# Kernel tuning notes

Hardware: AMD Instinct MI355X
Metric: run time of the kernel (lower is better)

Reference implementation:

```python
import jax, jax.numpy as jnp
import numpy as np

N = 100000   # nodes
E = 1000000  # edges
F_IN = 64    # input node features
EMB = 32     # init_emb
C = 32       # hidden/out channels per head
H = 4        # heads
HC = H * C   # 128
NEG_SLOPE = 0.2


def setup_inputs() -> dict:
    key = jax.random.key(0)
    ks = jax.random.split(key, 40)
    g = lambda k, shape: jax.random.normal(k, shape, jnp.float32) * 0.05
    inp = {
        "x": jax.random.normal(ks[0], (N, F_IN), jnp.float32),
        "edge_index": jax.random.randint(ks[1], (2, E), 0, N, jnp.int32),
        "W0": g(ks[2], (F_IN, EMB)),
    }
    i = 3
    for p, din in (("f", EMB), ("m", HC), ("l", HC)):
        inp[p + "_Wl"] = g(ks[i], (din, HC)); i += 1
        inp[p + "_bl"] = g(ks[i], (HC,));     i += 1
        inp[p + "_Wr"] = g(ks[i], (din, HC)); i += 1
        inp[p + "_br"] = g(ks[i], (HC,));     i += 1
        inp[p + "_att"] = g(ks[i], (H, C));   i += 1
        inp[p + "_cb"] = g(ks[i], (HC,));     i += 1
        inp[p + "_Ws"] = g(ks[i], (din, HC)); i += 1
        inp[p + "_bs"] = g(ks[i], (HC,));     i += 1
    return inp


def _gatv2(x, src, dst, Wl, bl, Wr, br, att, cb):
    # GATv2Conv, bipartite weights, concat heads, add_self_loops=False
    xl = (x @ Wl + bl).reshape(-1, H, C)  # source transform [N,H,C]
    xr = (x @ Wr + br).reshape(-1, H, C)  # target transform [N,H,C]
    e = xl[src] + xr[dst]                 # [E,H,C]
    s = jnp.where(e > 0, e, NEG_SLOPE * e)
    score = jnp.einsum('ehc,hc->eh', s, att)  # [E,H]
    mmax = jax.ops.segment_max(score, dst, num_segments=N)
    ex = jnp.exp(score - mmax[dst])
    den = jax.ops.segment_sum(ex, dst, num_segments=N)
    alpha = ex / den[dst]                 # segment softmax over in-edges
    out = jax.ops.segment_sum(xl[src] * alpha[:, :, None], dst, num_segments=N)
    return out.reshape(-1, HC) + cb


def reference(x, edge_index,
              W0,
              f_Wl, f_bl, f_Wr, f_br, f_att, f_cb, f_Ws, f_bs,
              m_Wl, m_bl, m_Wr, m_br, m_att, m_cb, m_Ws, m_bs,
              l_Wl, l_bl, l_Wr, l_br, l_att, l_cb, l_Ws, l_bs):
    src, dst = edge_index[0], edge_index[1]
    h = jax.nn.relu(x @ W0)
    h = jax.nn.relu(_gatv2(h, src, dst, f_Wl, f_bl, f_Wr, f_br, f_att, f_cb) + h @ f_Ws + f_bs)
    for _ in range(3):  # conv_mid / lin_mid weights are SHARED across the 3 iterations
        h = jax.nn.relu(_gatv2(h, src, dst, m_Wl, m_bl, m_Wr, m_br, m_att, m_cb) + h @ m_Ws + m_bs)
    h = _gatv2(h, src, dst, l_Wl, l_bl, l_Wr, l_br, l_att, l_cb) + h @ l_Ws + l_bs
    h = h / jnp.linalg.norm(h, axis=-1, keepdims=True)
    return h
```

## Files before the change

### kernel.cpp

```cpp
#include <hip/hip_runtime.h>
#include <hip/hip_bf16.h>
#include <math.h>

#define N_NODES 100000
#define N_EDGES 1000000
#define NEG_SLOPE 0.2f
#define NBUCK 98
#define BSHIFT 10
#define SLAB 12288
#define BINA_EDGES 4096

typedef short v8s __attribute__((ext_vector_type(8)));
typedef float v4f __attribute__((ext_vector_type(4)));

__device__ inline unsigned pack_bf16(float a, float b) {
    unsigned ua = __float_as_uint(a);
    unsigned ub = __float_as_uint(b);
    ua = (ua + 0x7FFFu + ((ua >> 16) & 1u)) >> 16;
    ub = (ub + 0x7FFFu + ((ub >> 16) & 1u)) >> 16;
    return ua | (ub << 16);
}
__device__ inline unsigned short bf16_rn(float x) {
    unsigned u = __float_as_uint(x);
    u = (u + 0x7FFFu + ((u >> 16) & 1u)) >> 16;
    return (unsigned short)u;
}
__device__ inline void unpack8(uint4 u, float* f) {
    f[0] = __uint_as_float(u.x << 16); f[1] = __uint_as_float(u.x & 0xFFFF0000u);
    f[2] = __uint_as_float(u.y << 16); f[3] = __uint_as_float(u.y & 0xFFFF0000u);
    f[4] = __uint_as_float(u.z << 16); f[5] = __uint_as_float(u.z & 0xFFFF0000u);
    f[6] = __uint_as_float(u.w << 16); f[7] = __uint_as_float(u.w & 0xFFFF0000u);
}

__global__ void init_cursors(int* __restrict__ gcursor) {
    int t = blockIdx.x * blockDim.x + threadIdx.x;
    if (t < NBUCK) gcursor[t] = t * SLAB;
}

__global__ __launch_bounds__(256) void binA_kernel(
    const int* __restrict__ src, const int* __restrict__ dst,
    int* __restrict__ gcursor, int* __restrict__ tmp) {
    __shared__ int bstart[NBUCK];
    __shared__ int addrbase[NBUCK];
    __shared__ int bcur[NBUCK];
    __shared__ int s[256];
    __shared__ int staged_val[BINA_EDGES];
    __shared__ int staged_addr[BINA_EDGES];
    const int tid = threadIdx.x;
    const int base = blockIdx.x * BINA_EDGES;
    const int ecount = min(BINA_EDGES, N_EDGES - base);

    if (tid < NBUCK) bcur[tid] = 0;
    __syncthreads();
    for (int j = tid; j < ecount; j += 256) {
        int d = dst[base + j];
        atomicAdd(&bcur[d >> BSHIFT], 1);
    }
    __syncthreads();
    int own = (tid < NBUCK) ? bcur[tid] : 0;
    s[tid] = own;
    __syncthreads();
    for (int off = 1; off < 256; off <<= 1) {
        int u = (tid >= off) ? s[tid - off] : 0;
        __syncthreads();
        s[tid] += u;
        __syncthreads();
    }
    if (tid < NBUCK) {
        int excl = s[tid] - own;
        bstart[tid] = excl;
        int resv = atomicAdd(&gcursor[tid], own);
        addrbase[tid] = resv - excl;
    }
    __syncthreads();
    if (tid < NBUCK) bcur[tid] = bstart[tid];
    __syncthreads();
    for (int j = tid; j < ecount; j += 256) {
        int d = dst[base + j];
        int sr = src[base + j];
        int bk = d >> BSHIFT;
        int lpos = atomicAdd(&bcur[bk], 1);
        staged_val[lpos] = ((d & ((1 << BSHIFT) - 1)) << 17) | sr;
        staged_addr[lpos] = addrbase[bk] + lpos;
    }
    __syncthreads();
    for (int j = tid; j < ecount; j += 256)
        tmp[staged_addr[j]] = staged_val[j];
}

__global__ void bucket_scan(const int* __restrict__ gcursor, int* __restrict__ bbase,
                            int* __restrict__ row_ptr) {
    __shared__ int s[128];
    int t = threadIdx.x;
    int v = (t < NBUCK) ? (gcursor[t] - t * SLAB) : 0;
    s[t] = v;
    __syncthreads();
    for (int off = 1; off < 128; off <<= 1) {
        int u = (t >= off) ? s[t - off] : 0;
        __syncthreads();
        s[t] += u;
        __syncthreads();
    }
    if (t < NBUCK) bbase[t] = s[t] - v;
    if (t == 0) row_ptr[N_NODES] = N_EDGES;
}

__global__ __launch_bounds__(256) void binB_kernel(
    const int* __restrict__ tmp, const int* __restrict__ gcursor,
    const int* __restrict__ bbase, int* __restrict__ row_ptr,
    int* __restrict__ srcs) {
    __shared__ int hist[1024];
    __shared__ int tsum[256];
    const int b = blockIdx.x;
    const int tid = threadIdx.x;
    const int base = b * SLAB;
    const int cnt = gcursor[b] - base;
    const int node0 = b << BSHIFT;
    const int nodes_in = min(1024, N_NODES - node0);
    const int gb = bbase[b];

    for (int i = tid; i < 1024; i += 256) hist[i] = 0;
    __syncthreads();
    for (int i = tid; i < cnt; i += 256)
        atomicAdd(&hist[tmp[base + i] >> 17], 1);
    __syncthreads();
    int v[4], local = 0;
#pragma unroll
    for (int j = 0; j < 4; ++j) {
        v[j] = hist[tid * 4 + j];
        local += v[j];
    }
    tsum[tid] = local;
    __syncthreads();
    for (int off = 1; off < 256; off <<= 1) {
        int u = (tid >= off) ? tsum[tid - off] : 0;
        __syncthreads();
        tsum[tid] += u;
        __syncthreads();
    }
    int run = tsum[tid] - local;
#pragma unroll
    for (int j = 0; j < 4; ++j) {
        hist[tid * 4 + j] = run;
        run += v[j];
    }
    __syncthreads();
    for (int i = tid; i < nodes_in; i += 256)
        row_ptr[node0 + i] = gb + hist[i];
    __syncthreads();
    for (int i = tid; i < cnt; i += 256) {
        int e = tmp[base + i];
        int pos = atomicAdd(&hist[e >> 17], 1);
        srcs[gb + pos] = e & 0x1FFFF;
    }
}

template <int K>
__global__ void convert_w(const float* __restrict__ Wl, const float* __restrict__ Wr,
                          const float* __restrict__ Ws, unsigned short* __restrict__ wt) {
    int idx = blockIdx.x * blockDim.x + threadIdx.x;
    if (idx >= 384 * K) return;
    int n = idx / K;
    int k = idx - n * K;
    int sec = n >> 7;
    int nn = n & 127;
    const float* W = (sec == 0) ? Wl : (sec == 1) ? Wr : Ws;
    wt[idx] = bf16_rn(W[k * 128 + nn]);
}

__global__ void h0_kernel(const float* __restrict__ x, const float* __restrict__ W0,
                          unsigned short* __restrict__ h) {
    int tid = blockIdx.x * blockDim.x + threadIdx.x;
    int col = tid & 31;
    int row = tid >> 5;
    if (row >= N_NODES) return;
    const float* xr = x + row * 64;
    float acc = 0.f;
#pragma unroll
    for (int k = 0; k < 64; ++k) acc = fmaf(xr[k], W0[k * 32 + col], acc);
    h[row * 32 + col] = bf16_rn(fmaxf(acc, 0.f));
}

template <int K>
__global__ __launch_bounds__(256) void mm3_mfma(
    const unsigned short* __restrict__ A, const unsigned short* __restrict__ Wt,
    const float* __restrict__ bl, const float* __restrict__ br, const float* __restrict__ bs,
    const float* __restrict__ cb,
    unsigned short* __restrict__ xl_bf, unsigned short* __restrict__ xr_bf,
    unsigned short* __restrict__ sk_bf) {
    const int tid = threadIdx.x;
    const int wave = tid >> 6;
    const int lane = tid & 63;
    const int q = lane >> 4;
    const int li = lane & 15;
    const int r0 = blockIdx.x * 256 + wave * 64;
    constexpr int KS = K / 32;

    v8s a[4][KS];
#pragma unroll
    for (int mi = 0; mi < 4; ++mi) {
        int row = r0 + mi * 16 + li;
        row = row < N_NODES ? row : N_NODES - 1;
#pragma unroll
        for (int ks = 0; ks < KS; ++ks)
            a[mi][ks] = *(const v8s*)&A[(size_t)row * K + ks * 32 + q * 8];
    }

    for (int t = 0; t < 6; ++t) {
        const int sec = t >> 1;
        const int c0 = (t & 1) * 64;
        v4f acc[4][4];
#pragma unroll
        for (int mi = 0; mi < 4; ++mi)
#pragma unroll
            for (int ni = 0; ni < 4; ++ni) acc[mi][ni] = (v4f)(0.f);

#pragma unroll
        for (int ks = 0; ks < KS; ++ks) {
            v8s b[4];
#pragma unroll
            for (int ni = 0; ni < 4; ++ni) {
                int col = sec * 128 + c0 + ni * 16 + li;
                b[ni] = *(const v8s*)&Wt[(size_t)col * K + ks * 32 + q * 8];
            }
#pragma unroll
            for (int mi = 0; mi < 4; ++mi)
#pragma unroll
                for (int ni = 0; ni < 4; ++ni)
                    acc[mi][ni] = __builtin_amdgcn_mfma_f32_16x16x32_bf16(b[ni], a[mi][ks], acc[mi][ni], 0, 0, 0);
        }

        unsigned short* dstp = (sec == 0) ? xl_bf : (sec == 1) ? xr_bf : sk_bf;
#pragma unroll
        for (int ni = 0; ni < 4; ++ni) {
            int cbase = c0 + ni * 16 + q * 4;
            float4 b4;
            if (sec == 0) b4 = *(const float4*)&bl[cbase];
            else if (sec == 1) b4 = *(const float4*)&br[cbase];
            else {
                float4 t1 = *(const float4*)&bs[cbase];
                float4 t2 = *(const float4*)&cb[cbase];
                b4 = make_float4(t1.x + t2.x, t1.y + t2.y, t1.z + t2.z, t1.w + t2.w);
            }
#pragma unroll
            for (int mi = 0; mi < 4; ++mi) {
                int row = r0 + mi * 16 + li;
                if (row >= N_NODES) continue;
                v4f v = acc[mi][ni];
                uint2 pk;
                pk.x = pack_bf16(v[0] + b4.x, v[1] + b4.y);
                pk.y = pack_bf16(v[2] + b4.z, v[3] + b4.w);
                *(uint2*)&dstp[(size_t)row * 128 + cbase] = pk;
            }
        }
    }
}

__global__ __launch_bounds__(256) void agg_kernel(
    const uint4* __restrict__ xlb4, const uint4* __restrict__ xrb4,
    const uint4* __restrict__ skb4, const int* __restrict__ row_ptr,
    const int* __restrict__ srcs, const float* __restrict__ att,
    uint4* __restrict__ out_bf, float* __restrict__ out_f,
    int write_bf, int do_relu, int do_norm) {
    int n = (blockIdx.x * blockDim.x + threadIdx.x) >> 6;
    if (n >= N_NODES) return;
    int lane = threadIdx.x & 63;
    int g = lane >> 4, li = lane & 15;

    uint4 xru = xrb4[(size_t)n * 16 + li];
    float xr_f[8];
    unpack8(xru, xr_f);
    float at_f[8];
    *(float4*)&at_f[0] = *(const float4*)&att[li * 8];
    *(float4*)&at_f[4] = *(const float4*)&att[li * 8 + 4];

    float acc[8];
#pragma unroll
    for (int i = 0; i < 8; ++i) acc[i] = 0.f;
    float lsum = 0.f;

    int beg = row_ptr[n], end = row_ptr[n + 1];
    if (beg < end) {
        int e0 = beg + g;
        int idx = e0 < end ? e0 : end - 1;
        int s = srcs[idx];
        uint4 xp = xlb4[(size_t)s * 16 + li];
        for (int cb = beg; cb < end; cb += 4) {
            uint4 cur = xp;
            bool valid = (cb + g) < end;
            int en = cb + 4 + g;
            if (en < end) {
                int s2 = srcs[en];
                xp = xlb4[(size_t)s2 * 16 + li];
            }
            float xf[8];
            unpack8(cur, xf);
            float p = 0.f;
#pragma unroll
            for (int i = 0; i < 8; ++i) {
                float e_ = xf[i] + xr_f[i];
                float lk = fmaxf(e_, NEG_SLOPE * e_);
                p = fmaf(lk, at_f[i], p);
            }
            p += __shfl_xor(p, 1);
            p += __shfl_xor(p, 2);
            float w = valid ? __expf(p) : 0.f;
            lsum += w;
#pragma unroll
            for (int i = 0; i < 8; ++i) acc[i] = fmaf(xf[i], w, acc[i]);
        }
    }
#pragma unroll
    for (int i = 0; i < 8; ++i) {
        acc[i] += __shfl_xor(acc[i], 16);
        acc[i] += __shfl_xor(acc[i], 32);
    }
    lsum += __shfl_xor(lsum, 16);
    lsum += __shfl_xor(lsum, 32);

    float inv = (lsum > 0.f) ? 1.f / lsum : 0.f;
    uint4 sku = skb4[(size_t)n * 16 + li];
    float sk_f[8];
    unpack8(sku, sk_f);
    float o[8];
#pragma unroll
    for (int i = 0; i < 8; ++i) o[i] = fmaf(acc[i], inv, sk_f[i]);
    if (do_relu) {
#pragma unroll
        for (int i = 0; i < 8; ++i) o[i] = fmaxf(o[i], 0.f);
    }
    if (do_norm) {
        float ss = 0.f;
#pragma unroll
        for (int i = 0; i < 8; ++i) ss = fmaf(o[i], o[i], ss);
        ss += __shfl_xor(ss, 1);
        ss += __shfl_xor(ss, 2);
        ss += __shfl_xor(ss, 4);
        ss += __shfl_xor(ss, 8);
        float r = 1.0f / sqrtf(ss);
#pragma unroll
        for (int i = 0; i < 8; ++i) o[i] *= r;
    }
    if (g == 0) {
        if (write_bf) {
            uint4 pk;
            pk.x = pack_bf16(o[0], o[1]);
            pk.y = pack_bf16(o[2], o[3]);
            pk.z = pack_bf16(o[4], o[5]);
            pk.w = pack_bf16(o[6], o[7]);
            out_bf[(size_t)n * 16 + li] = pk;
        } else {
            *(float4*)&out_f[(size_t)n * 128 + li * 8] = make_float4(o[0], o[1], o[2], o[3]);
            *(float4*)&out_f[(size_t)n * 128 + li * 8 + 4] = make_float4(o[4], o[5], o[6], o[7]);
        }
    }
}

extern "C" void kernel_launch(void* const* d_in, const int* in_sizes, int n_in,
                              void* d_out, int out_size, void* d_ws, size_t ws_size,
                              hipStream_t stream) {
    const float* x = (const float*)d_in[0];
    const int* ei = (const int*)d_in[1];
    const int* src = ei;
    const int* dst = ei + N_EDGES;
    const float* W0 = (const float*)d_in[2];

    const float* f_p[8];
    const float* m_p[8];
    const float* l_p[8];
    for (int i = 0; i < 8; ++i) f_p[i] = (const float*)d_in[3 + i];
    for (int i = 0; i < 8; ++i) m_p[i] = (const float*)d_in[11 + i];
    for (int i = 0; i < 8; ++i) l_p[i] = (const float*)d_in[19 + i];

    char* ws = (char*)d_ws;
    unsigned short* xl_bf = (unsigned short*)ws; ws += (size_t)N_NODES * 128 * 2;
    unsigned short* xr_bf = (unsigned short*)ws; ws += (size_t)N_NODES * 128 * 2;
    unsigned short* sk_bf = (unsigned short*)ws; ws += (size_t)N_NODES * 128 * 2;
    unsigned short* h_bf = (unsigned short*)ws;  ws += (size_t)N_NODES * 128 * 2;
    int* row_ptr = (int*)ws;       ws += (size_t)(N_NODES + 1) * 4;
    int* srcs = (int*)ws;          ws += (size_t)N_EDGES * 4;
    int* tmp = (int*)ws;           ws += (size_t)NBUCK * SLAB * 4;
    int* gcursor = (int*)ws;       ws += (size_t)NBUCK * 4;
    int* bbase = (int*)ws;         ws += (size_t)NBUCK * 4;
    unsigned short* wt_f = (unsigned short*)ws; ws += (size_t)384 * 32 * 2;
    unsigned short* wt_m = (unsigned short*)ws; ws += (size_t)384 * 128 * 2;
    unsigned short* wt_l = (unsigned short*)ws; ws += (size_t)384 * 128 * 2;

    init_cursors<<<1, 128, 0, stream>>>(gcursor);
    binA_kernel<<<(N_EDGES + BINA_EDGES - 1) / BINA_EDGES, 256, 0, stream>>>(src, dst, gcursor, tmp);
    bucket_scan<<<1, 128, 0, stream>>>(gcursor, bbase, row_ptr);
    binB_kernel<<<NBUCK, 256, 0, stream>>>(tmp, gcursor, bbase, row_ptr, srcs);

    convert_w<32><<<(384 * 32 + 255) / 256, 256, 0, stream>>>(f_p[0], f_p[2], f_p[6], wt_f);
    convert_w<128><<<(384 * 128 + 255) / 256, 256, 0, stream>>>(m_p[0], m_p[2], m_p[6], wt_m);
    convert_w<128><<<(384 * 128 + 255) / 256, 256, 0, stream>>>(l_p[0], l_p[2], l_p[6], wt_l);

    h0_kernel<<<(N_NODES * 32) / 256, 256, 0, stream>>>(x, W0, h_bf);

    const int gmm = (N_NODES + 255) / 256;
    const int gagg = (N_NODES * 64) / 256;
    float* out = (float*)d_out;

    mm3_mfma<32><<<gmm, 256, 0, stream>>>(h_bf, wt_f, f_p[1], f_p[3], f_p[7], f_p[5],
                                          xl_bf, xr_bf, sk_bf);
    agg_kernel<<<gagg, 256, 0, stream>>>((uint4*)xl_bf, (uint4*)xr_bf, (uint4*)sk_bf,
                                         row_ptr, srcs, f_p[4],
                                         (uint4*)h_bf, nullptr, 1, 1, 0);

    for (int it = 0; it < 3; ++it) {
        mm3_mfma<128><<<gmm, 256, 0, stream>>>(h_bf, wt_m, m_p[1], m_p[3], m_p[7], m_p[5],
                                               xl_bf, xr_bf, sk_bf);
        agg_kernel<<<gagg, 256, 0, stream>>>((uint4*)xl_bf, (uint4*)xr_bf, (uint4*)sk_bf,
                                             row_ptr, srcs, m_p[4],
                                             (uint4*)h_bf, nullptr, 1, 1, 0);
    }

    mm3_mfma<128><<<gmm, 256, 0, stream>>>(h_bf, wt_l, l_p[1], l_p[3], l_p[7], l_p[5],
                                           xl_bf, xr_bf, sk_bf);
    agg_kernel<<<gagg, 256, 0, stream>>>((uint4*)xl_bf, (uint4*)xr_bf, (uint4*)sk_bf,
                                         row_ptr, srcs, l_p[4],
                                         nullptr, out, 0, 0, 1);
}
```

Measured before the change: 728.8 us.

## Deepen gather prefetch pipeline in aggregation and shrink GEMM blocks to one wave

Restructures the edge aggregation loop to keep three rounds of neighbor feature loads plus index loads in flight (12 edges ahead) instead of a single prefetch. It also rewrites the leaky-ReLU via an abs-based identity, scalarizes row_ptr reads with readfirstlane, hoists the skip-connection load, and adds an occupancy hint. The projection GEMM kernel is launched with 64-thread single-wave blocks for finer scheduling. The aim is to hide gather latency, which dominates the memory-bound aggregation. In exchange it needs more registers and may lower occupancy.

After: 685.9 us. -5.9%, faster.

```diff
diff --git a/kernel.cpp b/kernel.cpp
--- a/kernel.cpp
+++ b/kernel.cpp
@@ -182,18 +182,16 @@
 }
 
 template <int K>
-__global__ __launch_bounds__(256) void mm3_mfma(
+__global__ __launch_bounds__(64) void mm3_mfma(
     const unsigned short* __restrict__ A, const unsigned short* __restrict__ Wt,
     const float* __restrict__ bl, const float* __restrict__ br, const float* __restrict__ bs,
     const float* __restrict__ cb,
     unsigned short* __restrict__ xl_bf, unsigned short* __restrict__ xr_bf,
     unsigned short* __restrict__ sk_bf) {
-    const int tid = threadIdx.x;
-    const int wave = tid >> 6;
-    const int lane = tid & 63;
+    const int lane = threadIdx.x & 63;
     const int q = lane >> 4;
     const int li = lane & 15;
-    const int r0 = blockIdx.x * 256 + wave * 64;
+    const int r0 = blockIdx.x * 64;
     constexpr int KS = K / 32;
 
     v8s a[4][KS];
@@ -256,7 +254,32 @@
     }
 }
 
-__global__ __launch_bounds__(256) void agg_kernel(
+#define AGG_BODY(XC, SVC, CB)                                               \
+    {                                                                       \
+        float xf[8];                                                        \
+        unpack8(XC, xf);                                                    \
+        bool vld = (CB) + g < end;                                          \
+        if ((CB) + 12 < end) XC = xlb4[(size_t)SVC * 16 + li];              \
+        if ((CB) + 24 < end) {                                              \
+            int ii = (CB) + 24 + g;                                         \
+            SVC = srcs[ii < end ? ii : em1];                                \
+        }                                                                   \
+        float p1 = 0.f, p2 = 0.f;                                           \
+        _Pragma("unroll") for (int i = 0; i < 8; ++i) {                     \
+            float e_ = xf[i] + xr_f[i];                                     \
+            p1 = fmaf(e_, at_f[i], p1);                                     \
+            p2 = fmaf(fabsf(e_), at_f[i], p2);                              \
+        }                                                                   \
+        float p = fmaf(0.6f, p1, 0.4f * p2);                                \
+        p += __shfl_xor(p, 1);                                              \
+        p += __shfl_xor(p, 2);                                              \
+        float w = vld ? __expf(p) : 0.f;                                    \
+        lsum += w;                                                          \
+        _Pragma("unroll") for (int i = 0; i < 8; ++i)                       \
+            acc[i] = fmaf(xf[i], w, acc[i]);                                \
+    }
+
+__global__ __launch_bounds__(256, 7) void agg_kernel(
     const uint4* __restrict__ xlb4, const uint4* __restrict__ xrb4,
     const uint4* __restrict__ skb4, const int* __restrict__ row_ptr,
     const int* __restrict__ srcs, const float* __restrict__ att,
@@ -267,49 +290,42 @@
     int lane = threadIdx.x & 63;
     int g = lane >> 4, li = lane & 15;
 
+    const int beg = __builtin_amdgcn_readfirstlane(row_ptr[n]);
+    const int end = __builtin_amdgcn_readfirstlane(row_ptr[n + 1]);
+
     uint4 xru = xrb4[(size_t)n * 16 + li];
-    float xr_f[8];
-    unpack8(xru, xr_f);
+    uint4 sku = skb4[(size_t)n * 16 + li];
+
     float at_f[8];
     *(float4*)&at_f[0] = *(const float4*)&att[li * 8];
     *(float4*)&at_f[4] = *(const float4*)&att[li * 8 + 4];
+    float xr_f[8];
+    unpack8(xru, xr_f);
 
     float acc[8];
 #pragma unroll
     for (int i = 0; i < 8; ++i) acc[i] = 0.f;
     float lsum = 0.f;
 
-    int beg = row_ptr[n], end = row_ptr[n + 1];
     if (beg < end) {
-        int e0 = beg + g;
-        int idx = e0 < end ? e0 : end - 1;
-        int s = srcs[idx];
-        uint4 xp = xlb4[(size_t)s * 16 + li];
-        for (int cb = beg; cb < end; cb += 4) {
-            uint4 cur = xp;
-            bool valid = (cb + g) < end;
-            int en = cb + 4 + g;
-            if (en < end) {
-                int s2 = srcs[en];
-                xp = xlb4[(size_t)s2 * 16 + li];
-            }
-            float xf[8];
-            unpack8(cur, xf);
-            float p = 0.f;
-#pragma unroll
-            for (int i = 0; i < 8; ++i) {
-                float e_ = xf[i] + xr_f[i];
-                float lk = fmaxf(e_, NEG_SLOPE * e_);
-                p = fmaf(lk, at_f[i], p);
-            }
-            p += __shfl_xor(p, 1);
-            p += __shfl_xor(p, 2);
-            float w = valid ? __expf(p) : 0.f;
-            lsum += w;
-#pragma unroll
-            for (int i = 0; i < 8; ++i) acc[i] = fmaf(xf[i], w, acc[i]);
+        const int em1 = end - 1;
+#define SRC_AT(Q) ({ int _ii = beg + (Q) * 4 + g; srcs[_ii < end ? _ii : em1]; })
+        int sv0 = SRC_AT(0), sv1 = SRC_AT(1), sv2 = SRC_AT(2);
+        uint4 x0 = xlb4[(size_t)sv0 * 16 + li];
+        uint4 x1 = xlb4[(size_t)sv1 * 16 + li];
+        uint4 x2 = xlb4[(size_t)sv2 * 16 + li];
+        sv0 = SRC_AT(3);
+        sv1 = SRC_AT(4);
+        sv2 = SRC_AT(5);
+#undef SRC_AT
+
+        for (int cb = beg; cb < end; cb += 12) {
+            AGG_BODY(x0, sv0, cb)
+            if (cb + 4 < end) AGG_BODY(x1, sv1, cb + 4)
+            if (cb + 8 < end) AGG_BODY(x2, sv2, cb + 8)
         }
     }
+
 #pragma unroll
     for (int i = 0; i < 8; ++i) {
         acc[i] += __shfl_xor(acc[i], 16);
@@ -319,7 +335,6 @@
     lsum += __shfl_xor(lsum, 32);
 
     float inv = (lsum > 0.f) ? 1.f / lsum : 0.f;
-    uint4 sku = skb4[(size_t)n * 16 + li];
     float sk_f[8];
     unpack8(sku, sk_f);
     float o[8];
@@ -397,26 +412,26 @@
 
     h0_kernel<<<(N_NODES * 32) / 256, 256, 0, stream>>>(x, W0, h_bf);
 
-    const int gmm = (N_NODES + 255) / 256;
+    const int gmm = (N_NODES + 63) / 64;
     const int gagg = (N_NODES * 64) / 256;
     float* out = (float*)d_out;
 
-    mm3_mfma<32><<<gmm, 256, 0, stream>>>(h_bf, wt_f, f_p[1], f_p[3], f_p[7], f_p[5],
-                                          xl_bf, xr_bf, sk_bf);
+    mm3_mfma<32><<<gmm, 64, 0, stream>>>(h_bf, wt_f, f_p[1], f_p[3], f_p[7], f_p[5],
+                                         xl_bf, xr_bf, sk_bf);
     agg_kernel<<<gagg, 256, 0, stream>>>((uint4*)xl_bf, (uint4*)xr_bf, (uint4*)sk_bf,
                                          row_ptr, srcs, f_p[4],
                                          (uint4*)h_bf, nullptr, 1, 1, 0);
 
     for (int it = 0; it < 3; ++it) {
-        mm3_mfma<128><<<gmm, 256, 0, stream>>>(h_bf, wt_m, m_p[1], m_p[3], m_p[7], m_p[5],
-                                               xl_bf, xr_bf, sk_bf);
+        mm3_mfma<128><<<gmm, 64, 0, stream>>>(h_bf, wt_m, m_p[1], m_p[3], m_p[7], m_p[5],
+                                              xl_bf, xr_bf, sk_bf);
         agg_kernel<<<gagg, 256, 0, stream>>>((uint4*)xl_bf, (uint4*)xr_bf, (uint4*)sk_bf,
                                              row_ptr, srcs, m_p[4],
                                              (uint4*)h_bf, nullptr, 1, 1, 0);
     }
 
-    mm3_mfma<128><<<gmm, 256, 0, stream>>>(h_bf, wt_l, l_p[1], l_p[3], l_p[7], l_p[5],
-                                           xl_bf, xr_bf, sk_bf);
+    mm3_mfma<128><<<gmm, 64, 0, stream>>>(h_bf, wt_l, l_p[1], l_p[3], l_p[7], l_p[5],
+                                          xl_bf, xr_bf, sk_bf);
     agg_kernel<<<gagg, 256, 0, stream>>>((uint4*)xl_bf, (uint4*)xr_bf, (uint4*)sk_bf,
                                          row_ptr, srcs, l_p[4],
                                          nullptr, out, 0, 0, 1);
```
